# Kernel optimization log

Measured on AMD Instinct MI355X. Metric: run time of the kernel, lower is better.

Reference implementation:

```python
import jax, jax.numpy as jnp
import numpy as np

WIN = 8   # window size
NH = 8    # n_heads


def _rel_pos_index(w):
    # Standard Swin relative position index table: [w*w, w*w] in [0, (2w-1)^2)
    coords = jnp.stack(jnp.meshgrid(jnp.arange(w), jnp.arange(w), indexing='ij'))  # [2,w,w]
    coords = coords.reshape(2, -1)  # [2, w*w]
    rel = coords[:, :, None] - coords[:, None, :]  # [2, w*w, w*w]
    rel = rel.transpose(1, 2, 0) + (w - 1)
    return rel[..., 0] * (2 * w - 1) + rel[..., 1]  # [w*w, w*w]


def setup_inputs() -> dict:
    key = jax.random.key(0)
    ks = jax.random.split(key, 6)
    C = 256
    return {
        'xs1': jax.random.normal(ks[0], (8, 64, 64, C), jnp.float32),
        'xs2': jax.random.normal(ks[1], (8, 32, 32, C), jnp.float32),
        'xq': jax.random.normal(ks[2], (8, 1024, C), jnp.float32),
        'W_qkv': jax.random.normal(ks[3], (C, 3 * C), jnp.float32) * 0.02,
        'b_qkv': jnp.zeros((3 * C,), jnp.float32),
        'W_proj': jax.random.normal(ks[4], (C, C), jnp.float32) * 0.02,
        'b_proj': jnp.zeros((C,), jnp.float32),
        'rel_pos_table': jax.random.normal(ks[5], ((2 * WIN - 1) ** 2, NH), jnp.float32) * 0.02,
    }


def reference(xs1, xs2, xq, W_qkv, b_qkv, W_proj, b_proj, rel_pos_table):
    B, H11, W11, C = xs1.shape
    _, H12, W12, _ = xs2.shape
    L11, L12, L2 = H11 * W11, H12 * W12, xq.shape[1]
    w, nh = WIN, NH
    hd = C // nh
    inv_sqrt_hd = 1.0 / jnp.sqrt(jnp.float32(hd))

    # joint QKV projection over concatenated tokens
    xsq = jnp.concatenate([xs1.reshape(B, L11, C), xs2.reshape(B, L12, C), xq], axis=1)
    qkv = xsq @ W_qkv + b_qkv  # [B, L11+L12+L2, 3C]

    # ---- windowed self-attention on xs1 ----
    xs_qkv = qkv[:, :L11].reshape(B, H11 // w, w, W11 // w, w, 3 * C)
    xs_qkv = xs_qkv.transpose(0, 1, 3, 2, 4, 5).reshape(-1, w * w, 3, nh, hd)  # [Bw, w^2, 3, nh, hd]
    xs_qkv = xs_qkv.transpose(2, 0, 3, 1, 4)  # [3, Bw, nh, w^2, hd]
    q, k, v = xs_qkv[0] * inv_sqrt_hd, xs_qkv[1], xs_qkv[2]
    scores = jnp.einsum('bhqd,bhkd->bhqk', q, k)  # [Bw, nh, w^2, w^2]
    bias = rel_pos_table[_rel_pos_index(w)]  # [w^2, w^2, nh]
    scores = scores + bias.transpose(2, 0, 1)[None]
    # original code divides by sqrt(head_features) again after the q scale
    probs = jax.nn.softmax(scores * inv_sqrt_hd, axis=-1)
    xs_out = jnp.einsum('bhqk,bhkd->bhqd', probs, v)  # [Bw, nh, w^2, hd]
    xs_out = xs_out.transpose(0, 2, 1, 3).reshape(-1, w, w, C)
    # window reverse
    xs_out = xs_out.reshape(B, H11 // w, W11 // w, w, w, C)
    xs_out = xs_out.transpose(0, 1, 3, 2, 4, 5).reshape(B, L11, C)

    # ---- cross attention: xq queries attend to [xs2 kv ; xq kv] ----
    xq_qkv = qkv[:, L11 + L12:].reshape(B, L2, 3, nh, hd).transpose(2, 0, 3, 1, 4)  # [3,B,nh,L2,hd]
    xq_q, xq_k, xq_v = xq_qkv[0], xq_qkv[1], xq_qkv[2]
    xs2_qkv = qkv[:, L11:L11 + L12].reshape(B, L12, 3, nh, hd).transpose(2, 0, 3, 1, 4)
    k2 = jnp.concatenate([xs2_qkv[1], xq_k], axis=2)  # [B,nh,L12+L2,hd]
    v2 = jnp.concatenate([xs2_qkv[2], xq_v], axis=2)
    # NOTE: original does NOT apply q_scale here, only the /sqrt(hd) divide
    cscores = jnp.einsum('bhqd,bhkd->bhqk', xq_q, k2) * inv_sqrt_hd
    cprobs = jax.nn.softmax(cscores, axis=-1)
    xq_out = jnp.einsum('bhqk,bhkd->bhqd', cprobs, v2)  # [B,nh,L2,hd]
    xq_out = xq_out.transpose(0, 2, 1, 3).reshape(B, L2, C)

    out = jnp.concatenate([xs_out, xq_out], axis=1) @ W_proj + b_proj  # [B, L11+L2, C]
    return out
```

## Files before the change

### kernel.cpp

```cpp
#include <hip/hip_runtime.h>
#include <hip/hip_bf16.h>

typedef unsigned short u16;
typedef unsigned int u32;
typedef __attribute__((ext_vector_type(8))) __bf16 bf16x8;
typedef __attribute__((ext_vector_type(4))) float f32x4;

#define INV_HD  0.03125f
#define INV_SHD 0.17677669529663687f
#define LOG2E   1.4426950408889634f

__device__ __forceinline__ float b2f(u16 u) {
  union { u32 i; float f; } v; v.i = ((u32)u) << 16; return v.f;
}
__device__ __forceinline__ u16 f2b(float f) {
  union { float f; u32 i; } v; v.f = f;
  u32 x = v.i;
  return (u16)((x + 0x7fffu + ((x >> 16) & 1u)) >> 16);
}
__device__ __forceinline__ bf16x8 ld16(const u16* p) {
  return *reinterpret_cast<const bf16x8*>(p);
}
union U8 { bf16x8 v; u16 s[8]; };
__device__ __forceinline__ u32 cvtpk(float a, float b) {
  u32 r;
  asm("v_cvt_pk_bf16_f32 %0, %1, %2" : "=v"(r) : "v"(a), "v"(b));
  return r;
}
__device__ __forceinline__ float pl32add(float x) {
  union { float f; u32 u; } c; c.f = x;
  auto r = __builtin_amdgcn_permlane32_swap(c.u, c.u, false, false);
  union { u32 u; float f; } a, b; a.u = r[0]; b.u = r[1];
  return a.f + b.f;
}
__device__ __forceinline__ float pl16add(float x) {
#if __has_builtin(__builtin_amdgcn_permlane16_swap)
  union { float f; u32 u; } c; c.f = x;
  auto r = __builtin_amdgcn_permlane16_swap(c.u, c.u, false, false);
  union { u32 u; float f; } a, b; a.u = r[0]; b.u = r[1];
  return a.f + b.f;
#else
  return x + __shfl_xor(x, 16, 64);
#endif
}

__global__ __launch_bounds__(256) void kPrep(
    const float* __restrict__ xs1, const float* __restrict__ xs2, const float* __restrict__ xq,
    const float* __restrict__ Wqkv, const float* __restrict__ Wproj, const float* __restrict__ tblg,
    u16* __restrict__ Abf, u16* __restrict__ WTq, u16* __restrict__ WTp, u16* __restrict__ BiasC)
{
  const int bx = blockIdx.x, tid = threadIdx.x;
  if (bx < 6144) {
    int t = bx * 256 + tid;
    int row = t >> 5, c8 = (t & 31) * 8;
    int b = row / 6144, r = row - b * 6144;
    const float* src;
    if (r < 4096)      src = xs1 + ((size_t)b * 4096 + r) * 256;
    else if (r < 5120) src = xs2 + ((size_t)b * 1024 + (r - 4096)) * 256;
    else               src = xq  + ((size_t)b * 1024 + (r - 5120)) * 256;
    U8 u;
#pragma unroll
    for (int j = 0; j < 8; ++j) u.s[j] = f2b(src[c8 + j]);
    *reinterpret_cast<bf16x8*>(Abf + (size_t)row * 256 + c8) = u.v;
  } else if (bx < 6912) {
    int i = (bx - 6144) * 256 + tid;
    int n = i >> 8, k = i & 255;
    WTq[i] = f2b(Wqkv[(size_t)k * 768 + n]);
  } else if (bx < 7168) {
    int i = (bx - 6912) * 256 + tid;
    int n = i >> 8, k = i & 255;
    WTp[i] = f2b(Wproj[(size_t)k * 256 + n]);
  } else {
    int gid = (bx - 7168) * 256 + tid;
    int lane = gid & 63, t = gid >> 6;
    int h = t >> 4, qt = (t >> 2) & 3, kt = t & 3;
    int lr = lane & 15, kg = lane >> 4;
    int q = qt * 16 + lr;
    int qi = q >> 3, qj = q & 7;
    ushort4 out;
#pragma unroll
    for (int i = 0; i < 4; ++i) {
      int key = kt * 16 + kg * 4 + i;
      int ki = key >> 3, kj = key & 7;
      int idx = (qi - ki + 7) * 15 + (qj - kj + 7);
      ((u16*)&out)[i] = f2b(tblg[idx * 8 + h] * (INV_SHD * LOG2E));
    }
    *reinterpret_cast<ushort4*>(BiasC + (size_t)(t * 64 + lane) * 4) = out;
  }
}

__global__ __launch_bounds__(256, 3) void kQKV(
    const u16* __restrict__ Abf,
    const u16* __restrict__ WT, const float* __restrict__ bias,
    u16* __restrict__ qk, u16* __restrict__ VT, u16* __restrict__ VST)
{
  __shared__ u16 St[4][5120];
  const int tid = threadIdx.x;
  const int lane = tid & 63, wid = tid >> 6;
  const int lr = lane & 15, kg = lane >> 4;
  const int m0 = blockIdx.x * 128 + wid * 32;
  const int by = blockIdx.y;
  const int m0blk = blockIdx.x * 128;
  const int bb = m0blk / 6144, rloc = m0blk - bb * 6144;
  u16* S = St[wid];

  bf16x8 a[2][8];
#pragma unroll
  for (int mt = 0; mt < 2; ++mt) {
    const u16* asrc = Abf + (size_t)(m0 + mt * 16 + lr) * 256 + kg * 8;
#pragma unroll
    for (int ks = 0; ks < 8; ++ks) a[mt][ks] = ld16(asrc + ks * 32);
  }

  const int n0 = (by < 4) ? by * 128 : 512 + (by - 4) * 128;
  const u16* bcol0 = WT + (size_t)(n0 + lr) * 256 + kg * 8;

  bf16x8 bq[2][8];
#pragma unroll
  for (int ks = 0; ks < 8; ++ks) bq[0][ks] = ld16(bcol0 + ks * 32);

  if (by < 4) {
    const float qsc = (by < 2) ? (INV_SHD * LOG2E) : 1.f;
#pragma unroll
    for (int nt = 0; nt < 8; ++nt) {
      const int cur = nt & 1, nxt = cur ^ 1;
      if (nt + 1 < 8) {
        const u16* bp = bcol0 + (size_t)(nt + 1) * 16 * 256;
#pragma unroll
        for (int ks = 0; ks < 8; ++ks) bq[nxt][ks] = ld16(bp + ks * 32);
      }
      f32x4 acc0 = {0.f,0.f,0.f,0.f}, acc1 = {0.f,0.f,0.f,0.f};
#pragma unroll
      for (int ks = 0; ks < 8; ++ks) {
        acc0 = __builtin_amdgcn_mfma_f32_16x16x32_bf16(a[0][ks], bq[cur][ks], acc0, 0, 0, 0);
        acc1 = __builtin_amdgcn_mfma_f32_16x16x32_bf16(a[1][ks], bq[cur][ks], acc1, 0, 0, 0);
      }
      float bv = bias[n0 + nt * 16 + lr];
#pragma unroll
      for (int i = 0; i < 4; ++i) {
        S[(kg * 4 + i) * 136 + nt * 16 + lr]      = f2b((acc0[i] + bv) * qsc);
        S[(16 + kg * 4 + i) * 136 + nt * 16 + lr] = f2b((acc1[i] + bv) * qsc);
      }
    }
#pragma unroll
    for (int p = 0; p < 8; ++p) {
      bf16x8 v = *reinterpret_cast<const bf16x8*>(&S[(p * 4 + kg) * 136 + lr * 8]);
      *reinterpret_cast<bf16x8*>(qk + (size_t)(m0 + p * 4 + kg) * 512 + n0 + lr * 8) = v;
    }
  } else {
    const bool isWin = (rloc < 4096);
    u16* Vb = isWin ? (VST + (size_t)bb * 256 * 4096) : (VT + (size_t)bb * 256 * 2048);
    const int VS = isWin ? 4096 : 2048;
    const int tokbase = (isWin ? rloc : (rloc - 4096)) + wid * 32;
#pragma unroll
    for (int nt = 0; nt < 8; ++nt) {
      const int cur = nt & 1, nxt = cur ^ 1;
      if (nt + 1 < 8) {
        const u16* bp = bcol0 + (size_t)(nt + 1) * 16 * 256;
#pragma unroll
        for (int ks = 0; ks < 8; ++ks) bq[nxt][ks] = ld16(bp + ks * 32);
      }
      f32x4 acc0 = {0.f,0.f,0.f,0.f}, acc1 = {0.f,0.f,0.f,0.f};
#pragma unroll
      for (int ks = 0; ks < 8; ++ks) {
        acc0 = __builtin_amdgcn_mfma_f32_16x16x32_bf16(bq[cur][ks], a[0][ks], acc0, 0, 0, 0);
        acc1 = __builtin_amdgcn_mfma_f32_16x16x32_bf16(bq[cur][ks], a[1][ks], acc1, 0, 0, 0);
      }
      float4 bv4 = *reinterpret_cast<const float4*>(bias + n0 + nt * 16 + kg * 4);
      const float* bvp = (const float*)&bv4;
#pragma unroll
      for (int i = 0; i < 4; ++i) {
        int c = nt * 16 + kg * 4 + i;
        S[c * 40 + lr]      = f2b(acc0[i] + bvp[i]);
        S[c * 40 + 16 + lr] = f2b(acc1[i] + bvp[i]);
      }
    }
#pragma unroll
    for (int p = 0; p < 8; ++p) {
      bf16x8 v = *reinterpret_cast<const bf16x8*>(&S[(p * 16 + lr) * 40 + kg * 8]);
      *reinterpret_cast<bf16x8*>(
          Vb + (size_t)((by - 4) * 128 + p * 16 + lr) * VS + tokbase + kg * 8) = v;
    }
  }
}

__device__ __forceinline__ void selfQT(
    int qt, bf16x8 qfq, const bf16x8 (&kf)[4],
    const u16* __restrict__ BiasC, int h, int lane, int lr, int kg, u16* P)
{
  f32x4 st[4];
#pragma unroll
  for (int kt = 0; kt < 4; ++kt) {
    f32x4 z = {0.f,0.f,0.f,0.f};
    st[kt] = __builtin_amdgcn_mfma_f32_16x16x32_bf16(kf[kt], qfq, z, 0, 0, 0);
  }
  const float c0 = INV_SHD;
  float lsum = 0.f;
#pragma unroll
  for (int kt = 0; kt < 4; ++kt) {
    ushort4 bv = *reinterpret_cast<const ushort4*>(
        BiasC + (size_t)((h * 16 + qt * 4 + kt) * 64 + lane) * 4);
    st[kt][0] = exp2f(st[kt][0] * c0 + b2f(bv.x));
    st[kt][1] = exp2f(st[kt][1] * c0 + b2f(bv.y));
    st[kt][2] = exp2f(st[kt][2] * c0 + b2f(bv.z));
    st[kt][3] = exp2f(st[kt][3] * c0 + b2f(bv.w));
    lsum += st[kt][0] + st[kt][1] + st[kt][2] + st[kt][3];
  }
  lsum = pl16add(lsum);
  lsum = pl32add(lsum);
  float inv = 1.f / lsum;
#pragma unroll
  for (int kt = 0; kt < 4; ++kt) {
    u32 w0 = cvtpk(st[kt][0] * inv, st[kt][1] * inv);
    u32 w1 = cvtpk(st[kt][2] * inv, st[kt][3] * inv);
    *reinterpret_cast<uint2*>(&P[lr * 72 + kt * 16 + kg * 4]) = make_uint2(w0, w1);
  }
}

__device__ __forceinline__ void cload(
    const u16* __restrict__ kbase, const u16* __restrict__ vbase, int kc0, int lr, int kg,
    bf16x8 (&kf)[4], bf16x8 (&vf)[4])
{
#pragma unroll
  for (int kt = 0; kt < 4; ++kt)
    kf[kt] = ld16(kbase + (size_t)(kc0 + kt * 16 + lr) * 512);
#pragma unroll
  for (int ks = 0; ks < 2; ++ks) {
    vf[ks]     = ld16(vbase + (size_t)lr * 2048 + kc0 + ks * 32 + kg * 8);
    vf[2 + ks] = ld16(vbase + (size_t)(16 + lr) * 2048 + kc0 + ks * 32 + kg * 8);
  }
}

__device__ __forceinline__ void cstep(
    const bf16x8 (&kf)[4], const bf16x8 (&vf)[4], bf16x8 qf,
    u16* P, int lr, int kg, f32x4& o0, f32x4& o1, float& l)
{
  f32x4 st[4];
#pragma unroll
  for (int kt = 0; kt < 4; ++kt) {
    f32x4 z = {0.f,0.f,0.f,0.f};
    st[kt] = __builtin_amdgcn_mfma_f32_16x16x32_bf16(kf[kt], qf, z, 0, 0, 0);
  }
  float lsum = 0.f;
#pragma unroll
  for (int kt = 0; kt < 4; ++kt) {
    st[kt][0] = exp2f(st[kt][0]);
    st[kt][1] = exp2f(st[kt][1]);
    st[kt][2] = exp2f(st[kt][2]);
    st[kt][3] = exp2f(st[kt][3]);
    lsum += st[kt][0] + st[kt][1] + st[kt][2] + st[kt][3];
  }
  lsum = pl16add(lsum);
  l += pl32add(lsum);
#pragma unroll
  for (int kt = 0; kt < 4; ++kt) {
    u32 w0 = cvtpk(st[kt][0], st[kt][1]);
    u32 w1 = cvtpk(st[kt][2], st[kt][3]);
    *reinterpret_cast<uint2*>(&P[lr * 72 + kt * 16 + kg * 4]) = make_uint2(w0, w1);
  }
#pragma unroll
  for (int ks = 0; ks < 2; ++ks) {
    bf16x8 pf = ld16(P + lr * 72 + ks * 32 + kg * 8);
    o0 = __builtin_amdgcn_mfma_f32_16x16x32_bf16(pf, vf[ks],     o0, 0, 0, 0);
    o1 = __builtin_amdgcn_mfma_f32_16x16x32_bf16(pf, vf[2 + ks], o1, 0, 0, 0);
  }
}

__global__ __launch_bounds__(256) void kAttn(
    const u16* __restrict__ qk, const u16* __restrict__ BiasC,
    const u16* __restrict__ VST, const u16* __restrict__ VT,
    u16* __restrict__ X, u16* __restrict__ Opart, float* __restrict__ ML)
{
  __shared__ u16 Pl[4][2304];
  const int tid = threadIdx.x;
  const int lane = tid & 63, wid = tid >> 6;
  const int lr = lane & 15, kg = lane >> 4;
  const int bx = blockIdx.x;

  if (bx < 1024) {
    const int bh = bx & 63, b = bh >> 3, h = bh & 7;
    const int qy = (bx >> 6) & 7, s = bx >> 9;
    const int q0 = qy * 128 + wid * 16;
    const size_t qrow0 = (size_t)b * 6144 + 5120;
    const size_t krow0 = (size_t)b * 6144 + 4096;
    const u16* kbase = qk + ((s ? qrow0 : krow0) * 512) + 256 + h * 32 + kg * 8;
    const u16* vbase = VT + (size_t)bh * 32 * 2048 + s * 1024;
    u16* PA = Pl[wid];
    u16* PB = Pl[wid] + 1152;

    bf16x8 qfA = ld16(qk + (qrow0 + q0      + lr) * 512 + h * 32 + kg * 8);
    bf16x8 qfB = ld16(qk + (qrow0 + q0 + 64 + lr) * 512 + h * 32 + kg * 8);

    f32x4 oA0 = {0.f,0.f,0.f,0.f}, oA1 = {0.f,0.f,0.f,0.f};
    f32x4 oB0 = {0.f,0.f,0.f,0.f}, oB1 = {0.f,0.f,0.f,0.f};
    float lA = 0.f, lB = 0.f;

#pragma unroll 1
    for (int ck = 0; ck < 16; ++ck) {
      bf16x8 kf[4], vf[4];
      cload(kbase, vbase, ck * 64, lr, kg, kf, vf);
      cstep(kf, vf, qfA, PA, lr, kg, oA0, oA1, lA);
      cstep(kf, vf, qfB, PB, lr, kg, oB0, oB1, lB);
    }

    const size_t rowb = (size_t)(s * 64 + bh) * 1024;
#pragma unroll
    for (int i = 0; i < 4; ++i) {
      int qa = q0 + kg * 4 + i, qb = qa + 64;
      Opart[(rowb + qa) * 32 + lr]      = f2b(oA0[i]);
      Opart[(rowb + qa) * 32 + 16 + lr] = f2b(oA1[i]);
      Opart[(rowb + qb) * 32 + lr]      = f2b(oB0[i]);
      Opart[(rowb + qb) * 32 + 16 + lr] = f2b(oB1[i]);
    }
    if (kg == 0) {
      *reinterpret_cast<float2*>(ML + (rowb + q0 + lr) * 2)      = make_float2(0.f, lA);
      *reinterpret_cast<float2*>(ML + (rowb + q0 + 64 + lr) * 2) = make_float2(0.f, lB);
    }
  } else {
    const int bid = bx - 1024;
    const int w = bid >> 1;
    const int h = (bid & 1) * 4 + wid;
    const int b = w >> 6, wz = w & 63;
    const int wy = wz >> 3, wx = wz & 7;
    const size_t tokbase = (size_t)b * 6144 + wy * 512 + wx * 8;
    const size_t xbase   = (size_t)b * 5120 + wy * 512 + wx * 8;
    u16* P = Pl[wid];

    bf16x8 qf[4], kf[4];
#pragma unroll
    for (int t4 = 0; t4 < 4; ++t4) {
      int t = t4 * 16 + lr;
      size_t row = tokbase + (t >> 3) * 64 + (t & 7);
      const u16* p = qk + row * 512 + h * 32 + kg * 8;
      qf[t4] = ld16(p);
      kf[t4] = ld16(p + 256);
    }
    bf16x8 vf[2][2];
#pragma unroll
    for (int dt = 0; dt < 2; ++dt)
#pragma unroll
      for (int ks = 0; ks < 2; ++ks)
        vf[dt][ks] = ld16(VST + ((size_t)(b * 8 + h) * 32 + dt * 16 + lr) * 4096
                          + (wy * 8 + ks * 4 + kg) * 64 + wx * 8);

    f32x4 o[4][2] = {};
#pragma unroll
    for (int qt = 0; qt < 4; ++qt) {
      selfQT(qt, qf[qt], kf, BiasC, h, lane, lr, kg, P);
#pragma unroll
      for (int ks = 0; ks < 2; ++ks) {
        bf16x8 pf = ld16(P + lr * 72 + ks * 32 + kg * 8);
        o[qt][0] = __builtin_amdgcn_mfma_f32_16x16x32_bf16(pf, vf[0][ks], o[qt][0], 0, 0, 0);
        o[qt][1] = __builtin_amdgcn_mfma_f32_16x16x32_bf16(pf, vf[1][ks], o[qt][1], 0, 0, 0);
      }
    }
#pragma unroll
    for (int qt = 0; qt < 4; ++qt)
#pragma unroll
      for (int i = 0; i < 4; ++i) {
        int t = qt * 16 + kg * 4 + i;
        size_t xrow = xbase + (t >> 3) * 64 + (t & 7);
#pragma unroll
        for (int dt = 0; dt < 2; ++dt)
          X[xrow * 256 + h * 32 + dt * 16 + lr] = f2b(o[qt][dt][i]);
      }
  }
}

__global__ __launch_bounds__(256) void kComb(
    const u16* __restrict__ Opart, const float* __restrict__ ML, u16* __restrict__ X)
{
  int gid = blockIdx.x * 256 + threadIdx.x;
  int row = gid >> 2;
  int dp = (gid & 3) * 8;
  int bh = row >> 10, q = row & 1023;
  int b = bh >> 3, h = bh & 7;
  float2 ml0 = *reinterpret_cast<const float2*>(ML + (size_t)row * 2);
  float2 ml1 = *reinterpret_cast<const float2*>(ML + (size_t)(65536 + row) * 2);
  float ms = fmaxf(ml0.x, ml1.x);
  float f0 = exp2f(ml0.x - ms), f1 = exp2f(ml1.x - ms);
  float inv = 1.f / (ml0.y * f0 + ml1.y * f1);
  f0 *= inv; f1 *= inv;
  U8 a, c, r;
  a.v = ld16(Opart + (size_t)row * 32 + dp);
  c.v = ld16(Opart + ((size_t)(65536 + row) * 32 + dp));
#pragma unroll
  for (int j = 0; j < 8; ++j) r.s[j] = f2b(b2f(a.s[j]) * f0 + b2f(c.s[j]) * f1);
  size_t xrow = (size_t)b * 5120 + 4096 + q;
  *reinterpret_cast<bf16x8*>(X + xrow * 256 + h * 32 + dp) = r.v;
}

__global__ __launch_bounds__(256) void kProj(
    const u16* __restrict__ Xin, const u16* __restrict__ WT, const float* __restrict__ bias,
    float* __restrict__ out)
{
  const int tid = threadIdx.x;
  const int lane = tid & 63, wid = tid >> 6;
  const int lr = lane & 15, kg = lane >> 4;
  const int m0 = blockIdx.x * 128 + wid * 32;
  const int n0 = blockIdx.y * 128;
  bf16x8 a[2][8];
#pragma unroll
  for (int mt = 0; mt < 2; ++mt) {
    const u16* src = Xin + (size_t)(m0 + mt * 16 + lr) * 256 + kg * 8;
#pragma unroll
    for (int ks = 0; ks < 8; ++ks) a[mt][ks] = ld16(src + ks * 32);
  }
  for (int nt = 0; nt < 8; ++nt) {
    const int n = n0 + nt * 16;
    const u16* bp = WT + (size_t)(n + lr) * 256 + kg * 8;
    f32x4 acc0 = {0.f,0.f,0.f,0.f}, acc1 = {0.f,0.f,0.f,0.f};
#pragma unroll
    for (int ks = 0; ks < 8; ++ks) {
      bf16x8 bq = ld16(bp + ks * 32);
      acc0 = __builtin_amdgcn_mfma_f32_16x16x32_bf16(a[0][ks], bq, acc0, 0, 0, 0);
      acc1 = __builtin_amdgcn_mfma_f32_16x16x32_bf16(a[1][ks], bq, acc1, 0, 0, 0);
    }
    float bv = bias[n + lr];
#pragma unroll
    for (int i = 0; i < 4; ++i) {
      int r0 = m0 + kg * 4 + i;
      out[(size_t)r0 * 256 + n + lr]        = acc0[i] + bv;
      out[(size_t)(r0 + 16) * 256 + n + lr] = acc1[i] + bv;
    }
  }
}

extern "C" void kernel_launch(void* const* d_in, const int* in_sizes, int n_in,
                              void* d_out, int out_size, void* d_ws, size_t ws_size,
                              hipStream_t stream)
{
  const float* xs1   = (const float*)d_in[0];
  const float* xs2   = (const float*)d_in[1];
  const float* xq    = (const float*)d_in[2];
  const float* Wqkv  = (const float*)d_in[3];
  const float* bqkv  = (const float*)d_in[4];
  const float* Wproj = (const float*)d_in[5];
  const float* bproj = (const float*)d_in[6];
  const float* tbl   = (const float*)d_in[7];

  u16* ws  = (u16*)d_ws;
  u16* qk  = ws;
  u16* X   = qk + 25165824;
  u16* WTq = X + 10485760;
  u16* WTp = WTq + 196608;
  u16* VT  = WTp + 65536;
  u16* VST = VT + 4194304;

  u16*   BiasC = (u16*)d_out;
  float* ML    = (float*)((char*)d_out + 262144);
  u16*   Opart = (u16*)((char*)d_out + 1310720);
  u16*   Abf   = (u16*)((char*)d_out + 10485760);

  kPrep<<<7200, 256, 0, stream>>>(xs1, xs2, xq, Wqkv, Wproj, tbl, Abf, WTq, WTp, BiasC);
  kQKV<<<dim3(384, 6), 256, 0, stream>>>(Abf, WTq, bqkv, qk, VT, VST);
  kAttn<<<2048, 256, 0, stream>>>(qk, BiasC, VST, VT, X, Opart, ML);
  kComb<<<1024, 256, 0, stream>>>(Opart, ML, X);
  kProj<<<dim3(320, 2), 256, 0, stream>>>(X, WTp, bproj, (float*)d_out);
}
```

Baseline: 216.7 us.

## Widen QKV GEMM blocks to 256 output columns with chunked LDS staging

Each kQKV block now computes 256 output columns (16 n-tiles) instead of 128, halving the grid in y so every A-row fragment loaded into registers is reused across twice as many columns. Shared-memory staging is cut by flushing results every 4 n-tiles (64 columns) instead of all at once, and launch bounds are raised to 4 blocks per CU. The n-tile loop is no longer unrolled, which adds loop overhead and dynamic indexing in exchange for lower register and LDS pressure. Fewer blocks also means less parallelism across the grid.

```diff
diff --git a/kernel.cpp b/kernel.cpp
--- a/kernel.cpp
+++ b/kernel.cpp
@@ -89,17 +89,16 @@
   }
 }
 
-__global__ __launch_bounds__(256, 3) void kQKV(
+__global__ __launch_bounds__(256, 4) void kQKV(
     const u16* __restrict__ Abf,
     const u16* __restrict__ WT, const float* __restrict__ bias,
     u16* __restrict__ qk, u16* __restrict__ VT, u16* __restrict__ VST)
 {
-  __shared__ u16 St[4][5120];
+  __shared__ u16 St[4][3072];
   const int tid = threadIdx.x;
   const int lane = tid & 63, wid = tid >> 6;
   const int lr = lane & 15, kg = lane >> 4;
   const int m0 = blockIdx.x * 128 + wid * 32;
-  const int by = blockIdx.y;
   const int m0blk = blockIdx.x * 128;
   const int bb = m0blk / 6144, rloc = m0blk - bb * 6144;
   u16* S = St[wid];
@@ -112,20 +111,27 @@
     for (int ks = 0; ks < 8; ++ks) a[mt][ks] = ld16(asrc + ks * 32);
   }
 
-  const int n0 = (by < 4) ? by * 128 : 512 + (by - 4) * 128;
-  const u16* bcol0 = WT + (size_t)(n0 + lr) * 256 + kg * 8;
-
+  const bool isWin = (rloc < 4096);
+  u16* Vb = isWin ? (VST + (size_t)bb * 256 * 4096) : (VT + (size_t)bb * 256 * 2048);
+  const int VS = isWin ? 4096 : 2048;
+  const int tokbase = (isWin ? rloc : (rloc - 4096)) + wid * 32;
+
+  const int g0 = blockIdx.y * 16;
   bf16x8 bq[2][8];
-#pragma unroll
-  for (int ks = 0; ks < 8; ++ks) bq[0][ks] = ld16(bcol0 + ks * 32);
-
-  if (by < 4) {
-    const float qsc = (by < 2) ? (INV_SHD * LOG2E) : 1.f;
-#pragma unroll
-    for (int nt = 0; nt < 8; ++nt) {
-      const int cur = nt & 1, nxt = cur ^ 1;
-      if (nt + 1 < 8) {
-        const u16* bp = bcol0 + (size_t)(nt + 1) * 16 * 256;
+  {
+    const u16* bp = WT + (size_t)(g0 * 16 + lr) * 256 + kg * 8;
+#pragma unroll
+    for (int ks = 0; ks < 8; ++ks) bq[0][ks] = ld16(bp + ks * 32);
+  }
+
+  if (blockIdx.y < 2) {
+    const float qsc = (blockIdx.y == 0) ? (INV_SHD * LOG2E) : 1.f;
+#pragma unroll 1
+    for (int t = 0; t < 16; ++t) {
+      const int g = g0 + t;
+      const int cur = t & 1, nxt = cur ^ 1;
+      if (t + 1 < 16) {
+        const u16* bp = WT + (size_t)((g + 1) * 16 + lr) * 256 + kg * 8;
 #pragma unroll
         for (int ks = 0; ks < 8; ++ks) bq[nxt][ks] = ld16(bp + ks * 32);
       }
@@ -135,28 +141,30 @@
         acc0 = __builtin_amdgcn_mfma_f32_16x16x32_bf16(a[0][ks], bq[cur][ks], acc0, 0, 0, 0);
         acc1 = __builtin_amdgcn_mfma_f32_16x16x32_bf16(a[1][ks], bq[cur][ks], acc1, 0, 0, 0);
       }
-      float bv = bias[n0 + nt * 16 + lr];
+      float bv = bias[g * 16 + lr];
+      const int tc = (t & 3) * 16;
 #pragma unroll
       for (int i = 0; i < 4; ++i) {
-        S[(kg * 4 + i) * 136 + nt * 16 + lr]      = f2b((acc0[i] + bv) * qsc);
-        S[(16 + kg * 4 + i) * 136 + nt * 16 + lr] = f2b((acc1[i] + bv) * qsc);
-      }
-    }
-#pragma unroll
-    for (int p = 0; p < 8; ++p) {
-      bf16x8 v = *reinterpret_cast<const bf16x8*>(&S[(p * 4 + kg) * 136 + lr * 8]);
-      *reinterpret_cast<bf16x8*>(qk + (size_t)(m0 + p * 4 + kg) * 512 + n0 + lr * 8) = v;
+        S[(kg * 4 + i) * 72 + tc + lr]        = f2b((acc0[i] + bv) * qsc);
+        S[(16 + kg * 4 + i) * 72 + tc + lr]   = f2b((acc1[i] + bv) * qsc);
+      }
+      if ((t & 3) == 3) {
+        const int cb = (g - 3) * 16;
+#pragma unroll
+        for (int s = 0; s < 4; ++s) {
+          int row = s * 8 + (lane >> 3), col = (lane & 7) * 8;
+          bf16x8 v = *reinterpret_cast<const bf16x8*>(&S[row * 72 + col]);
+          *reinterpret_cast<bf16x8*>(qk + (size_t)(m0 + row) * 512 + cb + col) = v;
+        }
+      }
     }
   } else {
-    const bool isWin = (rloc < 4096);
-    u16* Vb = isWin ? (VST + (size_t)bb * 256 * 4096) : (VT + (size_t)bb * 256 * 2048);
-    const int VS = isWin ? 4096 : 2048;
-    const int tokbase = (isWin ? rloc : (rloc - 4096)) + wid * 32;
-#pragma unroll
-    for (int nt = 0; nt < 8; ++nt) {
-      const int cur = nt & 1, nxt = cur ^ 1;
-      if (nt + 1 < 8) {
-        const u16* bp = bcol0 + (size_t)(nt + 1) * 16 * 256;
+#pragma unroll 1
+    for (int t = 0; t < 16; ++t) {
+      const int g = g0 + t;
+      const int cur = t & 1, nxt = cur ^ 1;
+      if (t + 1 < 16) {
+        const u16* bp = WT + (size_t)((g + 1) * 16 + lr) * 256 + kg * 8;
 #pragma unroll
         for (int ks = 0; ks < 8; ++ks) bq[nxt][ks] = ld16(bp + ks * 32);
       }
@@ -166,20 +174,24 @@
         acc0 = __builtin_amdgcn_mfma_f32_16x16x32_bf16(bq[cur][ks], a[0][ks], acc0, 0, 0, 0);
         acc1 = __builtin_amdgcn_mfma_f32_16x16x32_bf16(bq[cur][ks], a[1][ks], acc1, 0, 0, 0);
       }
-      float4 bv4 = *reinterpret_cast<const float4*>(bias + n0 + nt * 16 + kg * 4);
+      float4 bv4 = *reinterpret_cast<const float4*>(bias + g * 16 + kg * 4);
       const float* bvp = (const float*)&bv4;
 #pragma unroll
       for (int i = 0; i < 4; ++i) {
-        int c = nt * 16 + kg * 4 + i;
+        int c = (t & 3) * 16 + kg * 4 + i;
         S[c * 40 + lr]      = f2b(acc0[i] + bvp[i]);
         S[c * 40 + 16 + lr] = f2b(acc1[i] + bvp[i]);
       }
-    }
-#pragma unroll
-    for (int p = 0; p < 8; ++p) {
-      bf16x8 v = *reinterpret_cast<const bf16x8*>(&S[(p * 16 + lr) * 40 + kg * 8]);
-      *reinterpret_cast<bf16x8*>(
-          Vb + (size_t)((by - 4) * 128 + p * 16 + lr) * VS + tokbase + kg * 8) = v;
+      if ((t & 3) == 3) {
+        const int cb = (g - 3) * 16 - 512;
+#pragma unroll
+        for (int pp = 0; pp < 4; ++pp) {
+          int c = pp * 16 + lr;
+          bf16x8 v = *reinterpret_cast<const bf16x8*>(&S[c * 40 + kg * 8]);
+          *reinterpret_cast<bf16x8*>(
+              Vb + (size_t)(cb + c) * VS + tokbase + kg * 8) = v;
+        }
+      }
     }
   }
 }
@@ -453,7 +465,7 @@
   u16*   Abf   = (u16*)((char*)d_out + 10485760);
 
   kPrep<<<7200, 256, 0, stream>>>(xs1, xs2, xq, Wqkv, Wproj, tbl, Abf, WTq, WTp, BiasC);
-  kQKV<<<dim3(384, 6), 256, 0, stream>>>(Abf, WTq, bqkv, qk, VT, VST);
+  kQKV<<<dim3(384, 3), 256, 0, stream>>>(Abf, WTq, bqkv, qk, VT, VST);
   kAttn<<<2048, 256, 0, stream>>>(qk, BiasC, VST, VT, X, Opart, ML);
   kComb<<<1024, 256, 0, stream>>>(Opart, ML, X);
   kProj<<<dim3(320, 2), 256, 0, stream>>>(X, WTp, bproj, (float*)d_out);
```

Measured after the change: 343.5 us. 58.5% more time.
